# Optimization experiments

Measured on AMD Instinct MI355X. Metric: run time of the kernel, lower is better.

## Reference

```python
import jax, jax.numpy as jnp
import numpy as np

N_CHUNKS = 2


def _sig_kernel(X, Y):
    """Signature kernel PDE solution K[:, -1, -1].
    X: (A, M, D), Y: (A, N, D). Effective grid is (M, N) (the original CUDA
    kernel's last row/col read OOB and are trimmed away).
    Recurrence: K[i,j] = K[i-1,j] + K[i,j-1] + K[i-1,j-1]*(inc[i-1,j-1]-1),
    K[0,:] = K[:,0] = 1.  For a fixed row i this is a cumulative sum:
    K[i,j] = 1 + cumsum_j( K[i-1,j] + K[i-1,j-1]*(inc-1) ).
    """
    dX = X[:, 1:] - X[:, :-1]                      # (A, M-1, D)
    dY = Y[:, 1:] - Y[:, :-1]                      # (A, N-1, D)
    inc = jnp.einsum('amd,and->amn', dX, dY)       # (A, M-1, N-1)
    n = inc.shape[2]
    dtype = inc.dtype

    def solve(inc_b):                              # inc_b: (M-1, N-1)
        row0 = jnp.ones(n + 1, dtype)

        def step(prev_row, inc_row):
            # c[j] = K[i-1,j+1] + K[i-1,j]*(inc[j]-1),  j = 0..n-1
            c = prev_row[1:] + prev_row[:-1] * (inc_row - 1.0)
            new_row = jnp.concatenate(
                [jnp.ones((1,), dtype), 1.0 + jnp.cumsum(c)])
            return new_row, None

        last_row, _ = jax.lax.scan(step, row0, inc_b)
        return last_row[-1]

    return jax.vmap(solve)(inc)                    # (A,)


def _sig_distance(x, y):
    return jnp.mean(_sig_kernel(x, x) + _sig_kernel(y, y)
                    - 2.0 * _sig_kernel(x, y))


def _sig_loss(X, Y, n_chunks=N_CHUNKS):
    if n_chunks == 1:
        return _sig_distance(X, Y)
    dist = jnp.zeros((), X.dtype)
    for k in range(2, n_chunks + 1):
        Xc = jnp.array_split(X, k, axis=1)
        Yc = jnp.array_split(Y, k, axis=1)
        for x1, x2, y1, y2 in zip(Xc[:-1], Xc[1:], Yc[:-1], Yc[1:]):
            dist = dist + _sig_distance(jnp.concatenate([x1, x2], axis=1),
                                        jnp.concatenate([y1, y2], axis=1))
    return dist


def setup_inputs() -> dict:
    key = jax.random.key(0)
    kx, ky = jax.random.split(key)
    A, L, D = 256, 256, 32
    SCALE = 0.02  # keep exp growth of the PDE solution in fp32 range
    X = SCALE * jax.random.normal(kx, (A, L, D), dtype=jnp.float32)
    Y = SCALE * jax.random.normal(ky, (A, L, D), dtype=jnp.float32)
    return {"X": X, "Y": Y}


def reference(X, Y):
    return _sig_loss(X, Y, n_chunks=N_CHUNKS)
```

## Files before the change

kernel.cpp:

```cpp
#include <hip/hip_runtime.h>


typedef _Float16 half8 __attribute__((ext_vector_type(8)));
typedef float f32x4_t __attribute__((ext_vector_type(4)));
typedef unsigned int u32x4 __attribute__((ext_vector_type(4)));

#define DPP_ADD(v, ctrl, rmask)                                               \
    ((v) + __int_as_float(__builtin_amdgcn_update_dpp(                        \
               0, __float_as_int(v), (ctrl), (rmask), 0xF, true)))

#define INV2048 4.8828125e-4f

__global__ __launch_bounds__(64)
__attribute__((amdgpu_waves_per_eu(1, 1)))
void sig_pde(const float* __restrict__ X,
             const float* __restrict__ Y,
             float* __restrict__ partial) {
    const int bid = blockIdx.x;
    const int p = bid >> 8;
    const int a = bid & 255;
    const float* __restrict__ U = (p == 1) ? Y : X;
    const float* __restrict__ V = (p == 0) ? X : Y;
    U += (size_t)a * 256 * 32;
    V += (size_t)a * 256 * 32;
    const int lane = threadIdx.x;
    const int m16 = lane & 15;
    const int g2 = (lane >> 4) * 2;

    __shared__ __attribute__((aligned(16))) u32x4 bH[16 * 64];
    __shared__ __attribute__((aligned(16))) u32x4 bL[16 * 64];
    __shared__ __attribute__((aligned(16))) float incL[16 * 260];

    const float4* U4 = (const float4*)U;
    const float4* V4 = (const float4*)V;

#pragma unroll 2
    for (int t = 0; t < 16; ++t) {
        int col = t * 16 + m16;
        int cp = (col + 1 < 256) ? col + 1 : 255;
        float4 lo0 = V4[col * 8 + g2], lo1 = V4[col * 8 + g2 + 1];
        float4 hi0 = V4[cp * 8 + g2],  hi1 = V4[cp * 8 + g2 + 1];
        float d[8] = {hi0.x - lo0.x, hi0.y - lo0.y, hi0.z - lo0.z, hi0.w - lo0.w,
                      hi1.x - lo1.x, hi1.y - lo1.y, hi1.z - lo1.z, hi1.w - lo1.w};
        half8 bh, bl;
#pragma unroll
        for (int i = 0; i < 8; ++i) {
            _Float16 h = (_Float16)d[i];
            bh[i] = h;
            bl[i] = (_Float16)((d[i] - (float)h) * 2048.0f);
        }
        bH[t * 64 + lane] = __builtin_bit_cast(u32x4, bh);
        bL[t * 64 + lane] = __builtin_bit_cast(u32x4, bl);
    }

    float kp0 = 1.0f, kp1 = 1.0f, kp2 = 1.0f, kp3 = 1.0f;

    auto loadA = [&](int blk, float4 (&dst)[4]) {
        int r0 = blk * 16 + m16;
        int r1 = (r0 + 1 < 256) ? r0 + 1 : 255;
        dst[0] = U4[r0 * 8 + g2];
        dst[1] = U4[r0 * 8 + g2 + 1];
        dst[2] = U4[r1 * 8 + g2];
        dst[3] = U4[r1 * 8 + g2 + 1];
    };

    auto scan_row = [&](float4 mv) {
        float kn = __int_as_float(__builtin_amdgcn_update_dpp(
            0, __float_as_int(kp0), 0x130 , 0xF, 0xF, true));
        float c0 = fmaf(kp0, mv.x, kp1);
        float c1 = fmaf(kp1, mv.y, kp2);
        float c2 = fmaf(kp2, mv.z, kp3);
        float c3 = (lane == 63) ? 0.0f : fmaf(kp3, mv.w, kn);
        float L0 = c0, L1 = L0 + c1, L2 = L1 + c2;
        float T = L2 + c3;
        float S = T;
        S = DPP_ADD(S, 0x111, 0xF);
        S = DPP_ADD(S, 0x112, 0xF);
        S = DPP_ADD(S, 0x114, 0xF);
        S = DPP_ADD(S, 0x118, 0xF);
        S = DPP_ADD(S, 0x142, 0xA);
        S = DPP_ADD(S, 0x143, 0xC);
        float E = S - T;
        kp0 = 1.0f + E;
        kp1 = 1.0f + E + L0;
        kp2 = 1.0f + E + L1;
        kp3 = 1.0f + E + L2;
    };

    const float4* rp = (const float4*)incL;
#define RD(Gv, r) Gv = rp[(r) * 65 + lane]
    auto scan16 = [&](bool full) {
        float4 ga0, ga1, ga2, ga3, gb0, gb1, gb2, gb3;
        RD(ga0, 0); RD(ga1, 1); RD(ga2, 2); RD(ga3, 3);
        RD(gb0, 4); RD(gb1, 5); RD(gb2, 6); RD(gb3, 7);
        scan_row(ga0); scan_row(ga1); scan_row(ga2); scan_row(ga3);
        RD(ga0, 8); RD(ga1, 9); RD(ga2, 10); RD(ga3, 11);
        scan_row(gb0); scan_row(gb1); scan_row(gb2); scan_row(gb3);
        RD(gb0, 12); RD(gb1, 13); RD(gb2, 14);
        if (full) RD(gb3, 15);
        scan_row(ga0); scan_row(ga1); scan_row(ga2); scan_row(ga3);
        scan_row(gb0); scan_row(gb1); scan_row(gb2);
        if (full) scan_row(gb3);
    };
#undef RD

    auto mfma_block = [&](const float4 (&src)[4]) {
        float d[8] = {src[2].x - src[0].x, src[2].y - src[0].y,
                      src[2].z - src[0].z, src[2].w - src[0].w,
                      src[3].x - src[1].x, src[3].y - src[1].y,
                      src[3].z - src[1].z, src[3].w - src[1].w};
        half8 ah, al;
#pragma unroll
        for (int i = 0; i < 8; ++i) {
            _Float16 h = (_Float16)d[i];
            ah[i] = h;
            al[i] = (_Float16)((d[i] - (float)h) * 2048.0f);
        }
        const f32x4_t zero4 = {0.0f, 0.0f, 0.0f, 0.0f};
        const f32x4_t mone4 = {-1.0f, -1.0f, -1.0f, -1.0f};
        const int rb = (lane >> 4) << 2;
#pragma unroll
        for (int t = 0; t < 16; ++t) {
            half8 bh = __builtin_bit_cast(half8, bH[t * 64 + lane]);
            half8 bl = __builtin_bit_cast(half8, bL[t * 64 + lane]);
            f32x4_t acc2 =
                __builtin_amdgcn_mfma_f32_16x16x32_f16(ah, bl, zero4, 0, 0, 0);
            acc2 = __builtin_amdgcn_mfma_f32_16x16x32_f16(al, bh, acc2, 0, 0, 0);
            f32x4_t acc1 =
                __builtin_amdgcn_mfma_f32_16x16x32_f16(ah, bh, mone4, 0, 0, 0);
            int cc = t * 16 + m16;
            incL[(rb + 0) * 260 + cc] = fmaf(acc2[0], INV2048, acc1[0]);
            incL[(rb + 1) * 260 + cc] = fmaf(acc2[1], INV2048, acc1[1]);
            incL[(rb + 2) * 260 + cc] = fmaf(acc2[2], INV2048, acc1[2]);
            incL[(rb + 3) * 260 + cc] = fmaf(acc2[3], INV2048, acc1[3]);
        }
    };

    float4 A[4];
    loadA(0, A);
    mfma_block(A);
#pragma clang loop unroll(disable)
    for (int b = 1; b < 16; ++b) {
        loadA(b, A);
        scan16(true);
        mfma_block(A);
    }
    scan16(false);

    if (lane == 63) {
        partial[bid] = (p == 2 ? -2.0f : 1.0f) * kp3;
    }
}

__global__ __launch_bounds__(256) void sig_reduce(const float* __restrict__ partial,
                                                  float* __restrict__ out) {
    const int t = threadIdx.x;
    float v = partial[t] + partial[t + 256] + partial[t + 512];
#pragma unroll
    for (int ofs = 32; ofs > 0; ofs >>= 1) v += __shfl_down(v, ofs);
    __shared__ float ws[4];
    if ((t & 63) == 0) ws[t >> 6] = v;
    __syncthreads();
    if (t == 0) out[0] = (ws[0] + ws[1] + ws[2] + ws[3]) * (1.0f / 256.0f);
}

extern "C" void kernel_launch(void* const* d_in, const int* in_sizes, int n_in,
                              void* d_out, int out_size, void* d_ws, size_t ws_size,
                              hipStream_t stream) {
    const float* X = (const float*)d_in[0];
    const float* Y = (const float*)d_in[1];
    float* partial = (float*)d_ws;
    sig_pde<<<dim3(768), dim3(64), 0, stream>>>(X, Y, partial);
    sig_reduce<<<dim3(1), dim3(256), 0, stream>>>(partial, (float*)d_out);
}
```

Before: 44.30 us.

## Interleave MFMA tiles with scan rows to overlap matrix and VALU work

Loads all 16 increment rows for the current block into registers up front, then interleaves the serial DPP scan rows with MFMA tile computations for the next block, instead of running the full scan and then the full MFMA block. This is meant to hide MFMA latency and LDS stores behind the latency-bound scan chain within a single wave. It raises register pressure (16 float4 values held live). There is also a possible hazard: MFMA tile stores write incL rows that the same wave reads for the current block, and correctness depends on every read being issued before those stores.

```diff
diff --git a/kernel.cpp b/kernel.cpp
--- a/kernel.cpp
+++ b/kernel.cpp
@@ -64,6 +64,19 @@
         dst[3] = U4[r1 * 8 + g2 + 1];
     };
 
+    auto makeAhAl = [&](const float4 (&src)[4], half8& ah, half8& al) {
+        float d[8] = {src[2].x - src[0].x, src[2].y - src[0].y,
+                      src[2].z - src[0].z, src[2].w - src[0].w,
+                      src[3].x - src[1].x, src[3].y - src[1].y,
+                      src[3].z - src[1].z, src[3].w - src[1].w};
+#pragma unroll
+        for (int i = 0; i < 8; ++i) {
+            _Float16 h = (_Float16)d[i];
+            ah[i] = h;
+            al[i] = (_Float16)((d[i] - (float)h) * 2048.0f);
+        }
+    };
+
     auto scan_row = [&](float4 mv) {
         float kn = __int_as_float(__builtin_amdgcn_update_dpp(
             0, __float_as_int(kp0), 0x130 , 0xF, 0xF, true));
@@ -87,65 +100,67 @@
         kp3 = 1.0f + E + L2;
     };
 
+    const f32x4_t zero4 = {0.0f, 0.0f, 0.0f, 0.0f};
+    const f32x4_t mone4 = {-1.0f, -1.0f, -1.0f, -1.0f};
+    const int rb = (lane >> 4) << 2;
+
+    auto mfma_tile = [&](int t, const half8& ah, const half8& al) {
+        half8 bh = __builtin_bit_cast(half8, bH[t * 64 + lane]);
+        half8 bl = __builtin_bit_cast(half8, bL[t * 64 + lane]);
+        f32x4_t acc2 =
+            __builtin_amdgcn_mfma_f32_16x16x32_f16(ah, bl, zero4, 0, 0, 0);
+        acc2 = __builtin_amdgcn_mfma_f32_16x16x32_f16(al, bh, acc2, 0, 0, 0);
+        f32x4_t acc1 =
+            __builtin_amdgcn_mfma_f32_16x16x32_f16(ah, bh, mone4, 0, 0, 0);
+        int cc = t * 16 + m16;
+        incL[(rb + 0) * 260 + cc] = fmaf(acc2[0], INV2048, acc1[0]);
+        incL[(rb + 1) * 260 + cc] = fmaf(acc2[1], INV2048, acc1[1]);
+        incL[(rb + 2) * 260 + cc] = fmaf(acc2[2], INV2048, acc1[2]);
+        incL[(rb + 3) * 260 + cc] = fmaf(acc2[3], INV2048, acc1[3]);
+    };
+
     const float4* rp = (const float4*)incL;
-#define RD(Gv, r) Gv = rp[(r) * 65 + lane]
-    auto scan16 = [&](bool full) {
-        float4 ga0, ga1, ga2, ga3, gb0, gb1, gb2, gb3;
-        RD(ga0, 0); RD(ga1, 1); RD(ga2, 2); RD(ga3, 3);
-        RD(gb0, 4); RD(gb1, 5); RD(gb2, 6); RD(gb3, 7);
-        scan_row(ga0); scan_row(ga1); scan_row(ga2); scan_row(ga3);
-        RD(ga0, 8); RD(ga1, 9); RD(ga2, 10); RD(ga3, 11);
-        scan_row(gb0); scan_row(gb1); scan_row(gb2); scan_row(gb3);
-        RD(gb0, 12); RD(gb1, 13); RD(gb2, 14);
-        if (full) RD(gb3, 15);
-        scan_row(ga0); scan_row(ga1); scan_row(ga2); scan_row(ga3);
-        scan_row(gb0); scan_row(gb1); scan_row(gb2);
-        if (full) scan_row(gb3);
-    };
-#undef RD
-
-    auto mfma_block = [&](const float4 (&src)[4]) {
-        float d[8] = {src[2].x - src[0].x, src[2].y - src[0].y,
-                      src[2].z - src[0].z, src[2].w - src[0].w,
-                      src[3].x - src[1].x, src[3].y - src[1].y,
-                      src[3].z - src[1].z, src[3].w - src[1].w};
-        half8 ah, al;
-#pragma unroll
-        for (int i = 0; i < 8; ++i) {
-            _Float16 h = (_Float16)d[i];
-            ah[i] = h;
-            al[i] = (_Float16)((d[i] - (float)h) * 2048.0f);
-        }
-        const f32x4_t zero4 = {0.0f, 0.0f, 0.0f, 0.0f};
-        const f32x4_t mone4 = {-1.0f, -1.0f, -1.0f, -1.0f};
-        const int rb = (lane >> 4) << 2;
-#pragma unroll
-        for (int t = 0; t < 16; ++t) {
-            half8 bh = __builtin_bit_cast(half8, bH[t * 64 + lane]);
-            half8 bl = __builtin_bit_cast(half8, bL[t * 64 + lane]);
-            f32x4_t acc2 =
-                __builtin_amdgcn_mfma_f32_16x16x32_f16(ah, bl, zero4, 0, 0, 0);
-            acc2 = __builtin_amdgcn_mfma_f32_16x16x32_f16(al, bh, acc2, 0, 0, 0);
-            f32x4_t acc1 =
-                __builtin_amdgcn_mfma_f32_16x16x32_f16(ah, bh, mone4, 0, 0, 0);
-            int cc = t * 16 + m16;
-            incL[(rb + 0) * 260 + cc] = fmaf(acc2[0], INV2048, acc1[0]);
-            incL[(rb + 1) * 260 + cc] = fmaf(acc2[1], INV2048, acc1[1]);
-            incL[(rb + 2) * 260 + cc] = fmaf(acc2[2], INV2048, acc1[2]);
-            incL[(rb + 3) * 260 + cc] = fmaf(acc2[3], INV2048, acc1[3]);
-        }
-    };
 
     float4 A[4];
     loadA(0, A);
-    mfma_block(A);
+    {
+        half8 ah, al;
+        makeAhAl(A, ah, al);
+#pragma unroll
+        for (int t = 0; t < 16; ++t) mfma_tile(t, ah, al);
+    }
+
+#define RD(n) float4 w##n = rp[(n) * 65 + lane]
 #pragma clang loop unroll(disable)
     for (int b = 1; b < 16; ++b) {
         loadA(b, A);
-        scan16(true);
-        mfma_block(A);
+        RD(0); RD(1); RD(2); RD(3); RD(4); RD(5); RD(6); RD(7);
+        RD(8); RD(9); RD(10); RD(11); RD(12); RD(13); RD(14); RD(15);
+        half8 ah, al;
+        makeAhAl(A, ah, al);
+        scan_row(w0); scan_row(w1); scan_row(w2); scan_row(w3);
+        mfma_tile(0, ah, al); mfma_tile(1, ah, al);
+        mfma_tile(2, ah, al); mfma_tile(3, ah, al);
+        scan_row(w4); scan_row(w5); scan_row(w6); scan_row(w7);
+        mfma_tile(4, ah, al); mfma_tile(5, ah, al);
+        mfma_tile(6, ah, al); mfma_tile(7, ah, al);
+        scan_row(w8); scan_row(w9); scan_row(w10); scan_row(w11);
+        mfma_tile(8, ah, al); mfma_tile(9, ah, al);
+        mfma_tile(10, ah, al); mfma_tile(11, ah, al);
+        scan_row(w12); scan_row(w13); scan_row(w14); scan_row(w15);
+        mfma_tile(12, ah, al); mfma_tile(13, ah, al);
+        mfma_tile(14, ah, al); mfma_tile(15, ah, al);
     }
-    scan16(false);
+
+    {
+        RD(0); RD(1); RD(2); RD(3); RD(4); RD(5); RD(6); RD(7);
+        RD(8); RD(9); RD(10); RD(11); RD(12); RD(13); RD(14);
+        scan_row(w0); scan_row(w1); scan_row(w2); scan_row(w3);
+        scan_row(w4); scan_row(w5); scan_row(w6); scan_row(w7);
+        scan_row(w8); scan_row(w9); scan_row(w10); scan_row(w11);
+        scan_row(w12); scan_row(w13); scan_row(w14);
+    }
+#undef RD
 
     if (lane == 63) {
         partial[bid] = (p == 2 ? -2.0f : 1.0f) * kp3;
```

Result: no change. 43.62 us (-1.5%).

## Split MFMA producer and scan consumer into separate waves with double-buffered LDS

Applied to the files above, without the earlier changes.

The block grows to two waves. Wave 0 computes the 16x256 increment tiles with MFMA into a double-buffered LDS array, and wave 1 runs the serial DPP row-scan on the previous tile, with a barrier handshake each block. The B-operand staging is now split across both waves. This is meant to hide the tensor-core and LDS-store work behind the latency-bound scan instead of running them one after the other in a single wave. In exchange it uses more LDS per block and adds a per-block barrier, and it drops the waves_per_eu hint.

```diff
diff --git a/kernel.cpp b/kernel.cpp
--- a/kernel.cpp
+++ b/kernel.cpp
@@ -11,11 +11,9 @@
 
 #define INV2048 4.8828125e-4f
 
-__global__ __launch_bounds__(64)
-__attribute__((amdgpu_waves_per_eu(1, 1)))
-void sig_pde(const float* __restrict__ X,
-             const float* __restrict__ Y,
-             float* __restrict__ partial) {
+__global__ __launch_bounds__(128) void sig_pde(const float* __restrict__ X,
+                                               const float* __restrict__ Y,
+                                               float* __restrict__ partial) {
     const int bid = blockIdx.x;
     const int p = bid >> 8;
     const int a = bid & 255;
@@ -23,19 +21,22 @@
     const float* __restrict__ V = (p == 0) ? X : Y;
     U += (size_t)a * 256 * 32;
     V += (size_t)a * 256 * 32;
-    const int lane = threadIdx.x;
+    const int tid = threadIdx.x;
+    const int wid = tid >> 6;
+    const int lane = tid & 63;
     const int m16 = lane & 15;
     const int g2 = (lane >> 4) * 2;
 
     __shared__ __attribute__((aligned(16))) u32x4 bH[16 * 64];
     __shared__ __attribute__((aligned(16))) u32x4 bL[16 * 64];
-    __shared__ __attribute__((aligned(16))) float incL[16 * 260];
+    __shared__ __attribute__((aligned(16))) float incD[2][16 * 260];
 
     const float4* U4 = (const float4*)U;
     const float4* V4 = (const float4*)V;
 
 #pragma unroll 2
-    for (int t = 0; t < 16; ++t) {
+    for (int tt = 0; tt < 8; ++tt) {
+        int t = wid * 8 + tt;
         int col = t * 16 + m16;
         int cp = (col + 1 < 256) ? col + 1 : 255;
         float4 lo0 = V4[col * 8 + g2], lo1 = V4[col * 8 + g2 + 1];
@@ -52,103 +53,105 @@
         bH[t * 64 + lane] = __builtin_bit_cast(u32x4, bh);
         bL[t * 64 + lane] = __builtin_bit_cast(u32x4, bl);
     }
+    __syncthreads();
 
-    float kp0 = 1.0f, kp1 = 1.0f, kp2 = 1.0f, kp3 = 1.0f;
-
-    auto loadA = [&](int blk, float4 (&dst)[4]) {
-        int r0 = blk * 16 + m16;
-        int r1 = (r0 + 1 < 256) ? r0 + 1 : 255;
-        dst[0] = U4[r0 * 8 + g2];
-        dst[1] = U4[r0 * 8 + g2 + 1];
-        dst[2] = U4[r1 * 8 + g2];
-        dst[3] = U4[r1 * 8 + g2 + 1];
-    };
-
-    auto scan_row = [&](float4 mv) {
-        float kn = __int_as_float(__builtin_amdgcn_update_dpp(
-            0, __float_as_int(kp0), 0x130 , 0xF, 0xF, true));
-        float c0 = fmaf(kp0, mv.x, kp1);
-        float c1 = fmaf(kp1, mv.y, kp2);
-        float c2 = fmaf(kp2, mv.z, kp3);
-        float c3 = (lane == 63) ? 0.0f : fmaf(kp3, mv.w, kn);
-        float L0 = c0, L1 = L0 + c1, L2 = L1 + c2;
-        float T = L2 + c3;
-        float S = T;
-        S = DPP_ADD(S, 0x111, 0xF);
-        S = DPP_ADD(S, 0x112, 0xF);
-        S = DPP_ADD(S, 0x114, 0xF);
-        S = DPP_ADD(S, 0x118, 0xF);
-        S = DPP_ADD(S, 0x142, 0xA);
-        S = DPP_ADD(S, 0x143, 0xC);
-        float E = S - T;
-        kp0 = 1.0f + E;
-        kp1 = 1.0f + E + L0;
-        kp2 = 1.0f + E + L1;
-        kp3 = 1.0f + E + L2;
-    };
-
-    const float4* rp = (const float4*)incL;
-#define RD(Gv, r) Gv = rp[(r) * 65 + lane]
-    auto scan16 = [&](bool full) {
-        float4 ga0, ga1, ga2, ga3, gb0, gb1, gb2, gb3;
-        RD(ga0, 0); RD(ga1, 1); RD(ga2, 2); RD(ga3, 3);
-        RD(gb0, 4); RD(gb1, 5); RD(gb2, 6); RD(gb3, 7);
-        scan_row(ga0); scan_row(ga1); scan_row(ga2); scan_row(ga3);
-        RD(ga0, 8); RD(ga1, 9); RD(ga2, 10); RD(ga3, 11);
-        scan_row(gb0); scan_row(gb1); scan_row(gb2); scan_row(gb3);
-        RD(gb0, 12); RD(gb1, 13); RD(gb2, 14);
-        if (full) RD(gb3, 15);
-        scan_row(ga0); scan_row(ga1); scan_row(ga2); scan_row(ga3);
-        scan_row(gb0); scan_row(gb1); scan_row(gb2);
-        if (full) scan_row(gb3);
-    };
-#undef RD
-
-    auto mfma_block = [&](const float4 (&src)[4]) {
-        float d[8] = {src[2].x - src[0].x, src[2].y - src[0].y,
-                      src[2].z - src[0].z, src[2].w - src[0].w,
-                      src[3].x - src[1].x, src[3].y - src[1].y,
-                      src[3].z - src[1].z, src[3].w - src[1].w};
-        half8 ah, al;
-#pragma unroll
-        for (int i = 0; i < 8; ++i) {
-            _Float16 h = (_Float16)d[i];
-            ah[i] = h;
-            al[i] = (_Float16)((d[i] - (float)h) * 2048.0f);
-        }
+    if (wid == 0) {
+        auto loadA = [&](int blk, float4 (&dst)[4]) {
+            int r0 = blk * 16 + m16;
+            int r1 = (r0 + 1 < 256) ? r0 + 1 : 255;
+            dst[0] = U4[r0 * 8 + g2];
+            dst[1] = U4[r0 * 8 + g2 + 1];
+            dst[2] = U4[r1 * 8 + g2];
+            dst[3] = U4[r1 * 8 + g2 + 1];
+        };
         const f32x4_t zero4 = {0.0f, 0.0f, 0.0f, 0.0f};
         const f32x4_t mone4 = {-1.0f, -1.0f, -1.0f, -1.0f};
         const int rb = (lane >> 4) << 2;
+
+        float4 A[4];
+        loadA(0, A);
+#pragma clang loop unroll(disable)
+        for (int b = 0; b < 16; ++b) {
+            float d[8] = {A[2].x - A[0].x, A[2].y - A[0].y,
+                          A[2].z - A[0].z, A[2].w - A[0].w,
+                          A[3].x - A[1].x, A[3].y - A[1].y,
+                          A[3].z - A[1].z, A[3].w - A[1].w};
+            half8 ah, al;
 #pragma unroll
-        for (int t = 0; t < 16; ++t) {
-            half8 bh = __builtin_bit_cast(half8, bH[t * 64 + lane]);
-            half8 bl = __builtin_bit_cast(half8, bL[t * 64 + lane]);
-            f32x4_t acc2 =
-                __builtin_amdgcn_mfma_f32_16x16x32_f16(ah, bl, zero4, 0, 0, 0);
-            acc2 = __builtin_amdgcn_mfma_f32_16x16x32_f16(al, bh, acc2, 0, 0, 0);
-            f32x4_t acc1 =
-                __builtin_amdgcn_mfma_f32_16x16x32_f16(ah, bh, mone4, 0, 0, 0);
-            int cc = t * 16 + m16;
-            incL[(rb + 0) * 260 + cc] = fmaf(acc2[0], INV2048, acc1[0]);
-            incL[(rb + 1) * 260 + cc] = fmaf(acc2[1], INV2048, acc1[1]);
-            incL[(rb + 2) * 260 + cc] = fmaf(acc2[2], INV2048, acc1[2]);
-            incL[(rb + 3) * 260 + cc] = fmaf(acc2[3], INV2048, acc1[3]);
+            for (int i = 0; i < 8; ++i) {
+                _Float16 h = (_Float16)d[i];
+                ah[i] = h;
+                al[i] = (_Float16)((d[i] - (float)h) * 2048.0f);
+            }
+            if (b + 1 < 16) loadA(b + 1, A);
+            float* __restrict__ inc = incD[b & 1];
+#pragma unroll
+            for (int t = 0; t < 16; ++t) {
+                half8 bh = __builtin_bit_cast(half8, bH[t * 64 + lane]);
+                half8 bl = __builtin_bit_cast(half8, bL[t * 64 + lane]);
+                f32x4_t acc2 = __builtin_amdgcn_mfma_f32_16x16x32_f16(
+                    ah, bl, zero4, 0, 0, 0);
+                acc2 = __builtin_amdgcn_mfma_f32_16x16x32_f16(
+                    al, bh, acc2, 0, 0, 0);
+                f32x4_t acc1 = __builtin_amdgcn_mfma_f32_16x16x32_f16(
+                    ah, bh, mone4, 0, 0, 0);
+                int cc = t * 16 + m16;
+                inc[(rb + 0) * 260 + cc] = fmaf(acc2[0], INV2048, acc1[0]);
+                inc[(rb + 1) * 260 + cc] = fmaf(acc2[1], INV2048, acc1[1]);
+                inc[(rb + 2) * 260 + cc] = fmaf(acc2[2], INV2048, acc1[2]);
+                inc[(rb + 3) * 260 + cc] = fmaf(acc2[3], INV2048, acc1[3]);
+            }
+            __syncthreads();
         }
-    };
+    } else {
+        float kp0 = 1.0f, kp1 = 1.0f, kp2 = 1.0f, kp3 = 1.0f;
 
-    float4 A[4];
-    loadA(0, A);
-    mfma_block(A);
+        auto scan_row = [&](float4 mv) {
+            float kn = __int_as_float(__builtin_amdgcn_update_dpp(
+                0, __float_as_int(kp0), 0x130 , 0xF, 0xF, true));
+            float c0 = fmaf(kp0, mv.x, kp1);
+            float c1 = fmaf(kp1, mv.y, kp2);
+            float c2 = fmaf(kp2, mv.z, kp3);
+            float c3 = (lane == 63) ? 0.0f : fmaf(kp3, mv.w, kn);
+            float L0 = c0, L1 = L0 + c1, L2 = L1 + c2;
+            float T = L2 + c3;
+            float S = T;
+            S = DPP_ADD(S, 0x111, 0xF);
+            S = DPP_ADD(S, 0x112, 0xF);
+            S = DPP_ADD(S, 0x114, 0xF);
+            S = DPP_ADD(S, 0x118, 0xF);
+            S = DPP_ADD(S, 0x142, 0xA);
+            S = DPP_ADD(S, 0x143, 0xC);
+            float E = S - T;
+            kp0 = 1.0f + E;
+            kp1 = 1.0f + E + L0;
+            kp2 = 1.0f + E + L1;
+            kp3 = 1.0f + E + L2;
+        };
+
 #pragma clang loop unroll(disable)
-    for (int b = 1; b < 16; ++b) {
-        loadA(b, A);
-        scan16(true);
-        mfma_block(A);
-    }
-    scan16(false);
+        for (int b = 0; b < 16; ++b) {
+            __syncthreads();
+            const float4* rp = (const float4*)incD[b & 1];
+            bool full = (b < 15);
+            float4 ga0, ga1, ga2, ga3, gb0, gb1, gb2, gb3;
+#define RD(Gv, r) Gv = rp[(r) * 65 + lane]
+            RD(ga0, 0); RD(ga1, 1); RD(ga2, 2); RD(ga3, 3);
+            RD(gb0, 4); RD(gb1, 5); RD(gb2, 6); RD(gb3, 7);
+            scan_row(ga0); scan_row(ga1); scan_row(ga2); scan_row(ga3);
+            RD(ga0, 8); RD(ga1, 9); RD(ga2, 10); RD(ga3, 11);
+            scan_row(gb0); scan_row(gb1); scan_row(gb2); scan_row(gb3);
+            RD(gb0, 12); RD(gb1, 13); RD(gb2, 14);
+            if (full) RD(gb3, 15);
+            scan_row(ga0); scan_row(ga1); scan_row(ga2); scan_row(ga3);
+            scan_row(gb0); scan_row(gb1); scan_row(gb2);
+            if (full) scan_row(gb3);
+#undef RD
+        }
 
-    if (lane == 63) {
-        partial[bid] = (p == 2 ? -2.0f : 1.0f) * kp3;
+        if (lane == 63) {
+            partial[bid] = (p == 2 ? -2.0f : 1.0f) * kp3;
+        }
     }
 }
 
@@ -170,6 +173,6 @@
     const float* X = (const float*)d_in[0];
     const float* Y = (const float*)d_in[1];
     float* partial = (float*)d_ws;
-    sig_pde<<<dim3(768), dim3(64), 0, stream>>>(X, Y, partial);
+    sig_pde<<<dim3(768), dim3(128), 0, stream>>>(X, Y, partial);
     sig_reduce<<<dim3(1), dim3(256), 0, stream>>>(partial, (float*)d_out);
 }
```

Result: slower. 67.52 us (+52.4%).

## Keep B fragments in registers and double-buffer the inc tile in LDS

Applied to the files above, without the earlier changes.

The split-fp16 B operand fragments now live in registers (16 half8 hi/lo pairs per lane) instead of being stored to and reloaded from LDS on every block. The inc tile in LDS is double-buffered, so the MFMA for block b writes one buffer while the scan reads the previous one, which lets the compiler overlap the two. The cost is about 128 extra VGPRs, which is acceptable at one wave per EU but could cause spills, and LDS use rises for the second inc buffer.

```diff
diff --git a/kernel.cpp b/kernel.cpp
--- a/kernel.cpp
+++ b/kernel.cpp
@@ -3,7 +3,6 @@
 
 typedef _Float16 half8 __attribute__((ext_vector_type(8)));
 typedef float f32x4_t __attribute__((ext_vector_type(4)));
-typedef unsigned int u32x4 __attribute__((ext_vector_type(4)));
 
 #define DPP_ADD(v, ctrl, rmask)                                               \
     ((v) + __int_as_float(__builtin_amdgcn_update_dpp(                        \
@@ -27,14 +26,13 @@
     const int m16 = lane & 15;
     const int g2 = (lane >> 4) * 2;
 
-    __shared__ __attribute__((aligned(16))) u32x4 bH[16 * 64];
-    __shared__ __attribute__((aligned(16))) u32x4 bL[16 * 64];
-    __shared__ __attribute__((aligned(16))) float incL[16 * 260];
+    __shared__ __attribute__((aligned(16))) float incD[2][16 * 260];
 
     const float4* U4 = (const float4*)U;
     const float4* V4 = (const float4*)V;
 
-#pragma unroll 2
+    half8 bh[16], bl[16];
+#pragma unroll
     for (int t = 0; t < 16; ++t) {
         int col = t * 16 + m16;
         int cp = (col + 1 < 256) ? col + 1 : 255;
@@ -42,15 +40,12 @@
         float4 hi0 = V4[cp * 8 + g2],  hi1 = V4[cp * 8 + g2 + 1];
         float d[8] = {hi0.x - lo0.x, hi0.y - lo0.y, hi0.z - lo0.z, hi0.w - lo0.w,
                       hi1.x - lo1.x, hi1.y - lo1.y, hi1.z - lo1.z, hi1.w - lo1.w};
-        half8 bh, bl;
 #pragma unroll
         for (int i = 0; i < 8; ++i) {
             _Float16 h = (_Float16)d[i];
-            bh[i] = h;
-            bl[i] = (_Float16)((d[i] - (float)h) * 2048.0f);
+            bh[t][i] = h;
+            bl[t][i] = (_Float16)((d[i] - (float)h) * 2048.0f);
         }
-        bH[t * 64 + lane] = __builtin_bit_cast(u32x4, bh);
-        bL[t * 64 + lane] = __builtin_bit_cast(u32x4, bl);
     }
 
     float kp0 = 1.0f, kp1 = 1.0f, kp2 = 1.0f, kp3 = 1.0f;
@@ -87,9 +82,9 @@
         kp3 = 1.0f + E + L2;
     };
 
-    const float4* rp = (const float4*)incL;
 #define RD(Gv, r) Gv = rp[(r) * 65 + lane]
-    auto scan16 = [&](bool full) {
+    auto scan16 = [&](const float* buf, bool full) {
+        const float4* rp = (const float4*)buf;
         float4 ga0, ga1, ga2, ga3, gb0, gb1, gb2, gb3;
         RD(ga0, 0); RD(ga1, 1); RD(ga2, 2); RD(ga3, 3);
         RD(gb0, 4); RD(gb1, 5); RD(gb2, 6); RD(gb3, 7);
@@ -104,7 +99,7 @@
     };
 #undef RD
 
-    auto mfma_block = [&](const float4 (&src)[4]) {
+    auto mfma_block = [&](const float4 (&src)[4], float* __restrict__ buf) {
         float d[8] = {src[2].x - src[0].x, src[2].y - src[0].y,
                       src[2].z - src[0].z, src[2].w - src[0].w,
                       src[3].x - src[1].x, src[3].y - src[1].y,
@@ -121,31 +116,29 @@
         const int rb = (lane >> 4) << 2;
 #pragma unroll
         for (int t = 0; t < 16; ++t) {
-            half8 bh = __builtin_bit_cast(half8, bH[t * 64 + lane]);
-            half8 bl = __builtin_bit_cast(half8, bL[t * 64 + lane]);
             f32x4_t acc2 =
-                __builtin_amdgcn_mfma_f32_16x16x32_f16(ah, bl, zero4, 0, 0, 0);
-            acc2 = __builtin_amdgcn_mfma_f32_16x16x32_f16(al, bh, acc2, 0, 0, 0);
+                __builtin_amdgcn_mfma_f32_16x16x32_f16(ah, bl[t], zero4, 0, 0, 0);
+            acc2 = __builtin_amdgcn_mfma_f32_16x16x32_f16(al, bh[t], acc2, 0, 0, 0);
             f32x4_t acc1 =
-                __builtin_amdgcn_mfma_f32_16x16x32_f16(ah, bh, mone4, 0, 0, 0);
+                __builtin_amdgcn_mfma_f32_16x16x32_f16(ah, bh[t], mone4, 0, 0, 0);
             int cc = t * 16 + m16;
-            incL[(rb + 0) * 260 + cc] = fmaf(acc2[0], INV2048, acc1[0]);
-            incL[(rb + 1) * 260 + cc] = fmaf(acc2[1], INV2048, acc1[1]);
-            incL[(rb + 2) * 260 + cc] = fmaf(acc2[2], INV2048, acc1[2]);
-            incL[(rb + 3) * 260 + cc] = fmaf(acc2[3], INV2048, acc1[3]);
+            buf[(rb + 0) * 260 + cc] = fmaf(acc2[0], INV2048, acc1[0]);
+            buf[(rb + 1) * 260 + cc] = fmaf(acc2[1], INV2048, acc1[1]);
+            buf[(rb + 2) * 260 + cc] = fmaf(acc2[2], INV2048, acc1[2]);
+            buf[(rb + 3) * 260 + cc] = fmaf(acc2[3], INV2048, acc1[3]);
         }
     };
 
     float4 A[4];
     loadA(0, A);
-    mfma_block(A);
+    mfma_block(A, incD[0]);
 #pragma clang loop unroll(disable)
     for (int b = 1; b < 16; ++b) {
         loadA(b, A);
-        scan16(true);
-        mfma_block(A);
+        scan16(incD[(b - 1) & 1], true);
+        mfma_block(A, incD[b & 1]);
     }
-    scan16(false);
+    scan16(incD[1], false);
 
     if (lane == 63) {
         partial[bid] = (p == 2 ? -2.0f : 1.0f) * kp3;
```

Result: slower. 45.28 us (+2.2%).
